# Kernel optimization log

Measured on AMD Instinct MI355X. Metric: run time of the kernel, lower is better.

Reference implementation:

```python
import jax, jax.numpy as jnp
import numpy as np

# --- Cl(5,0) geometric algebra with 32 basis blades (bitmask representation) ---
def _cayley():
    def sgn(a, b):
        # sign from reordering basis vectors (Euclidean metric: no metric signs)
        a >>= 1
        s = 0
        while a:
            s += bin(a & b).count('1')
            a >>= 1
        return -1.0 if (s & 1) else 1.0
    C = np.zeros((32, 32, 32), np.float32)
    for i in range(32):
        for j in range(32):
            C[i, j, i ^ j] = sgn(i, j)
    return jnp.asarray(C)

CAYLEY = _cayley()  # [32,32,32] structure constants
EPS = 1e-8

def geometric_product(a, b):
    # a, b: [..., 32]
    return jnp.einsum('...i,...j,ijk->...k', a, b, CAYLEY)

def manifold_normalization(x):
    # project multivector back to the unit-norm manifold
    return x * jax.lax.rsqrt(jnp.sum(x * x, axis=-1, keepdims=True) + EPS)


def setup_inputs() -> dict:
    key = jax.random.key(0)
    k1, k2, k3 = jax.random.split(key, 3)
    B, S, N, D = 16, 256, 16, 6
    H = 16  # hidden_channels
    x = jax.random.normal(k1, (B, S, N, D), dtype=jnp.float32)
    W_in = jax.random.normal(k2, (D, H * 32), dtype=jnp.float32) * 0.1
    b_in = jnp.zeros((H * 32,), dtype=jnp.float32)
    W_out = jax.random.normal(k3, (H * 32, D), dtype=jnp.float32) * 0.05
    b_out = jnp.zeros((D,), dtype=jnp.float32)
    return {"x": x, "W_in": W_in, "b_in": b_in, "W_out": W_out, "b_out": b_out}


def reference(x, W_in, b_in, W_out, b_out):
    B, S, N, D = x.shape
    H = W_in.shape[1] // 32
    # proj_in over the whole sequence at once
    x_embs = (x @ W_in + b_in).reshape(B, S, N, H, 32)
    # psi init: identity rotor (scalar blade = 1)
    psi0 = jnp.zeros((B, N, H, 32), dtype=x.dtype).at[..., 0].set(1.0)

    def step(psi, inp):
        u_t, x_t = inp  # [B,N,H,32], [B,N,D]
        delta_r = manifold_normalization(u_t.at[..., 0].add(1.0))
        psi = manifold_normalization(geometric_product(delta_r, psi))
        pred_delta = psi.reshape(B, N, H * 32) @ W_out + b_out
        return psi, x_t + pred_delta

    _, ys = jax.lax.scan(step, psi0,
                         (jnp.swapaxes(x_embs, 0, 1), jnp.swapaxes(x, 0, 1)))
    return jnp.swapaxes(ys, 0, 1)  # [B,S,N,D]
```

## Files before the change

### kernel.cpp

```cpp
#include <hip/hip_runtime.h>


#define EPS 1e-8f

constexpr int pcnt(int v) { int s = 0; while (v) { s += v & 1; v >>= 1; } return s; }
constexpr int sgni(int a, int b) {
    a >>= 1; int s = 0;
    while (a) { s += pcnt(a & b); a >>= 1; }
    return (s & 1) ? -1 : 1;
}
struct El { int m; int s; };
constexpr El emul(El a, El b) { return { a.m ^ b.m, a.s * b.s * sgni(a.m, b.m) }; }

struct MTab {
    int mm[16]; int ms[16];
    int qi[4][4]; int qs[4][4];
    int sig[32];
    bool ok;
};
constexpr MTab mkMT() {
    MTab t{}; t.ok = true;
    El g0{17,1}, g1{18,1}, g2{20,1}, g3{24,1};
    El q1 = emul(g0, g1), q2 = emul(g1, g2);
    El q[4] = { El{0,1}, q1, q2, emul(q1, q2) };
    El u = emul(emul(g0, g1), emul(g2, g3));
    El v = emul(emul(g0, g1), g2);
    El mset[4] = { El{0,1}, u, v, emul(u, v) };
    {
        El c1 = emul(q[1], q[1]); if (!(c1.m == 0 && c1.s == -1)) t.ok = false;
        El c2 = emul(q[2], q[2]); if (!(c2.m == 0 && c2.s == -1)) t.ok = false;
        El c3 = emul(q[3], q[3]); if (!(c3.m == 0 && c3.s == -1)) t.ok = false;
        El c4 = emul(u, u); if (!(c4.m == 0 && c4.s == 1)) t.ok = false;
        El c5 = emul(v, v); if (!(c5.m == 0 && c5.s == 1)) t.ok = false;
        El c6 = emul(u, v), c7 = emul(v, u);
        if (!(c6.m == c7.m && c6.s == -c7.s)) t.ok = false;
        for (int i = 1; i < 4; ++i) {
            El a1 = emul(u, q[i]), a2 = emul(q[i], u);
            if (!(a1.m == a2.m && a1.s == a2.s)) t.ok = false;
            El b1 = emul(v, q[i]), b2 = emul(q[i], v);
            if (!(b1.m == b2.m && b1.s == b2.s)) t.ok = false;
        }
    }
    for (int tt = 0; tt < 4; ++tt)
        for (int a = 0; a < 4; ++a) {
            El e = emul(q[a], mset[tt]);
            t.mm[a + 4 * tt] = e.m; t.ms[a + 4 * tt] = e.s;
            if (pcnt(e.m) & 1) t.ok = false;
        }
    for (int i = 0; i < 16; ++i)
        for (int j = i + 1; j < 16; ++j)
            if (t.mm[i] == t.mm[j]) t.ok = false;
    for (int a = 0; a < 4; ++a)
        for (int b = 0; b < 4; ++b) {
            El e = emul(q[a], q[b]);
            int f = -1;
            for (int c = 0; c < 4; ++c) if (q[c].m == e.m) f = c;
            if (f < 0) { t.ok = false; f = 0; }
            t.qi[a][b] = f; t.qs[a][b] = e.s * q[f].s;
        }
    for (int m = 0; m < 32; ++m) t.sig[m] = sgni(m ^ 31, 31);
    return t;
}
__device__ constexpr MTab MT = mkMT();
static_assert(mkMT().ok, "Cl(5,0) = M2(H)+M2(H) derivation failed");

__global__ __launch_bounds__(256, 1) void k_prep(
        const float* __restrict__ W_in, const float* __restrict__ b_in,
        const float* __restrict__ W_out, float* __restrict__ WP) {
    const int idx = blockIdx.x * 256 + threadIdx.x;
    if (idx >= 6656) return;
    if (idx < 3584) {
        const int h = idx / 224, r = idx % 224;
        const int es = r / 112, r2 = r % 112;
        const float p = es ? -1.f : 1.f;
        const int c = (r2 < 96) ? (r2 & 15) : (r2 - 96);
        const int e = c >> 2, a = c & 3;
        const int base = (e == 0 || e == 3) ? 0 : 8;
        const float se = (e == 0 || e == 1) ? 1.f : -1.f;
        float val = 0.f;
        for (int k = 0; k < 2; ++k) {
            const int i = a + base + 4 * k;
            const float beta = k ? se : 1.f;
            const int m = MT.mm[i];
            const float s = (float)MT.ms[i];
            const float sg = (float)MT.sig[m];
            float wm, wn;
            if (r2 < 96) {
                const int d = r2 >> 4;
                wm = W_in[d * 512 + h * 32 + m];
                wn = W_in[d * 512 + h * 32 + (m ^ 31)];
            } else {
                wm = b_in[h * 32 + m];
                wn = b_in[h * 32 + (m ^ 31)];
            }
            val += beta * s * (wm + p * sg * wn);
        }
        WP[idx] = val;
    } else {
        const int j = idx - 3584;
        const int h = j / 192, r = j % 192;
        const int es = r / 96, r2 = r % 96;
        const float p = es ? -1.f : 1.f;
        const int c = r2 / 6, d = r2 % 6;
        const int e = c >> 2, a = c & 3;
        const int base = (e == 0 || e == 3) ? 0 : 8;
        const float se = (e == 0 || e == 1) ? 1.f : -1.f;
        float val = 0.f;
        for (int k = 0; k < 2; ++k) {
            const int i = a + base + 4 * k;
            const float beta = k ? se : 1.f;
            const int m = MT.mm[i];
            const float s = (float)MT.ms[i];
            const float sg = (float)MT.sig[m];
            const float wm = W_out[(h * 32 + m) * 6 + d];
            const float wn = W_out[(h * 32 + (m ^ 31)) * 6 + d];
            val += 0.25f * beta * s * (wm + p * sg * wn);
        }
        WP[idx] = val;
    }
}

__device__ __forceinline__ void build16(const float* __restrict__ Wsp,
                                        const float xv[6], float U[16]) {
#pragma unroll
    for (int c = 0; c < 16; ++c) U[c] = Wsp[96 + c];
#pragma unroll
    for (int d = 0; d < 6; ++d)
#pragma unroll
        for (int c = 0; c < 16; ++c)
            U[c] = fmaf(xv[d], Wsp[d * 16 + c], U[c]);
    U[0]  += 1.0f;
    U[12] += 1.0f;
}

__device__ __forceinline__ void hfma(float* __restrict__ z,
                                     const float* __restrict__ p,
                                     const float* __restrict__ q) {
#pragma unroll
    for (int a = 0; a < 4; ++a)
#pragma unroll
        for (int b = 0; b < 4; ++b)
            z[MT.qi[a][b]] = fmaf((float)MT.qs[a][b] * p[a], q[b], z[MT.qi[a][b]]);
}

__device__ __forceinline__ void gpm(float* __restrict__ Z,
                                    const float* __restrict__ U,
                                    const float* __restrict__ X) {
#pragma unroll
    for (int k = 0; k < 16; ++k) Z[k] = 0.f;
    hfma(Z + 0,  U + 0, X + 0);   hfma(Z + 0,  U + 4,  X + 8);
    hfma(Z + 4,  U + 0, X + 4);   hfma(Z + 4,  U + 4,  X + 12);
    hfma(Z + 8,  U + 8, X + 0);   hfma(Z + 8,  U + 12, X + 8);
    hfma(Z + 12, U + 8, X + 4);   hfma(Z + 12, U + 12, X + 12);
}

__device__ __forceinline__ float ssum32(const float* a, const float* b) {
    float s0 = 0.f, s1 = 0.f, s2 = 0.f, s3 = 0.f;
#pragma unroll
    for (int k = 0; k < 16; k += 4) {
        s0 = fmaf(a[k],     a[k],     s0); s1 = fmaf(a[k + 1], a[k + 1], s1);
        s2 = fmaf(a[k + 2], a[k + 2], s2); s3 = fmaf(a[k + 3], a[k + 3], s3);
        s0 = fmaf(b[k],     b[k],     s0); s1 = fmaf(b[k + 1], b[k + 1], s1);
        s2 = fmaf(b[k + 2], b[k + 2], s2); s3 = fmaf(b[k + 3], b[k + 3], s3);
    }
    return (s0 + s1) + (s2 + s3);
}

__global__ __launch_bounds__(256, 1) void k_fused(
        const float* __restrict__ x, const float* __restrict__ WP,
        float* __restrict__ WS4) {
    __shared__ float LP[4 * 8 * 64 * 6];

    const int tid  = threadIdx.x;
    const int lane = tid & 63;
    const int w    = __builtin_amdgcn_readfirstlane((int)(tid >> 6));
    const int hg   = blockIdx.x & 3;
    const int p    = blockIdx.x >> 2;
    const int h    = 4 * hg + w;
    const int sc   = lane & 31;
    const int bn = p * 2 + (lane >> 5), b = bn >> 4, n = bn & 15;
    const float* __restrict__ Wp0 = WP + h * 224;
    const float* __restrict__ Wp1 = WP + h * 224 + 112;
    const float* __restrict__ Op0 = WP + 3584 + h * 192;
    const float* __restrict__ Op1 = WP + 3584 + h * 192 + 96;

    float Xp[16], Xm[16];
    {
        const int t = sc * 8;
        const float2* xp = (const float2*)(x + ((b * 256 + t) * 16 + n) * 6);
        float2 x01 = xp[0], x23 = xp[1], x45 = xp[2];
        const float xv[6] = {x01.x, x01.y, x23.x, x23.y, x45.x, x45.y};
        build16(Wp0, xv, Xp);
        build16(Wp1, xv, Xm);
    }
    for (int i = 1; i < 8; ++i) {
        const int t = sc * 8 + i;
        const float2* xp = (const float2*)(x + ((b * 256 + t) * 16 + n) * 6);
        float2 x01 = xp[0], x23 = xp[1], x45 = xp[2];
        const float xv[6] = {x01.x, x01.y, x23.x, x23.y, x45.x, x45.y};
        float U[16], Z[16];
        build16(Wp0, xv, U);
        gpm(Z, U, Xp);
#pragma unroll
        for (int k = 0; k < 16; ++k) Xp[k] = Z[k];
        build16(Wp1, xv, U);
        gpm(Z, U, Xm);
#pragma unroll
        for (int k = 0; k < 16; ++k) Xm[k] = Z[k];
    }
    {
        float rs = rsqrtf(0.25f * ssum32(Xp, Xm) + EPS);
#pragma unroll
        for (int k = 0; k < 16; ++k) { Xp[k] *= rs; Xm[k] *= rs; }
    }

#pragma unroll
    for (int k = 1; k < 32; k <<= 1) {
        float prp[16], prm[16];
#pragma unroll
        for (int j = 0; j < 16; ++j) {
            prp[j] = __shfl_up(Xp[j], k, 32);
            prm[j] = __shfl_up(Xm[j], k, 32);
        }
        if (sc >= k) {
            float Z[16];
            gpm(Z, Xp, prp);
#pragma unroll
            for (int m = 0; m < 16; ++m) Xp[m] = Z[m];
            gpm(Z, Xm, prm);
#pragma unroll
            for (int m = 0; m < 16; ++m) Xm[m] = Z[m];
        }
    }
    {
        float rs = rsqrtf(0.25f * ssum32(Xp, Xm) + EPS);
#pragma unroll
        for (int j = 0; j < 16; ++j) { Xp[j] *= rs; Xm[j] *= rs; }
    }
    float Rp[16], Rm[16];
#pragma unroll
    for (int j = 0; j < 16; ++j) {
        Rp[j] = __shfl_up(Xp[j], 1, 32);
        Rm[j] = __shfl_up(Xm[j], 1, 32);
    }
    if (sc == 0) {
#pragma unroll
        for (int j = 0; j < 16; ++j) { Rp[j] = 0.0f; Rm[j] = 0.0f; }
        Rp[0] = 1.0f; Rp[12] = 1.0f;
        Rm[0] = 1.0f; Rm[12] = 1.0f;
    }

    for (int i = 0; i < 8; ++i) {
        const int t = sc * 8 + i;
        const float2* xp = (const float2*)(x + ((b * 256 + t) * 16 + n) * 6);
        float2 x01 = xp[0], x23 = xp[1], x45 = xp[2];
        const float xv[6] = {x01.x, x01.y, x23.x, x23.y, x45.x, x45.y};
        float U[16], Zp[16], Zm[16];
        build16(Wp0, xv, U);
        gpm(Zp, U, Rp);
        build16(Wp1, xv, U);
        gpm(Zm, U, Rm);
        float rs = rsqrtf(0.25f * ssum32(Zp, Zm) + EPS);
        float pd[6] = {0.f, 0.f, 0.f, 0.f, 0.f, 0.f};
#pragma unroll
        for (int c = 0; c < 16; ++c)
#pragma unroll
            for (int d = 0; d < 6; ++d) {
                pd[d] = fmaf(Zp[c], Op0[c * 6 + d], pd[d]);
                pd[d] = fmaf(Zm[c], Op1[c * 6 + d], pd[d]);
            }
#pragma unroll
        for (int k = 0; k < 16; ++k) { Rp[k] = Zp[k]; Rm[k] = Zm[k]; }
        float* lp = LP + ((w * 8 + i) * 64 + lane) * 6;
#pragma unroll
        for (int d = 0; d < 6; ++d) lp[d] = pd[d] * rs;
    }

    __syncthreads();

    float* outp = WS4 + (hg * 128 + p) * 3072;
    for (int s = tid; s < 3072; s += 256) {
        const int d = s % 6, tc = s / 6;
        const int c = tc & 1, t = tc >> 1;
        const int li = ((t & 7) * 64 + (c * 32 + (t >> 3))) * 6 + d;
        float acc = LP[0 * 3072 + li] + LP[1 * 3072 + li]
                  + LP[2 * 3072 + li] + LP[3 * 3072 + li];
        outp[s] = acc;
    }
}

__global__ __launch_bounds__(256, 1) void k_reduce(
        const float* __restrict__ x, const float* __restrict__ b_out,
        const float* __restrict__ WS4, float* __restrict__ out) {
    const int idx = blockIdx.x * 256 + threadIdx.x;
    const int p = idx / 3072, s = idx % 3072;
    const int d = s % 6, tc = s / 6;
    const int c = tc & 1, t = tc >> 1;
    const int bn = p * 2 + c, b = bn >> 4, n = bn & 15;
    const int o = ((b * 256 + t) * 16 + n) * 6 + d;
    float acc = x[o] + b_out[d];
#pragma unroll
    for (int hg = 0; hg < 4; ++hg)
        acc += WS4[(hg * 128 + p) * 3072 + s];
    out[o] = acc;
}

extern "C" void kernel_launch(void* const* d_in, const int* in_sizes, int n_in,
                              void* d_out, int out_size, void* d_ws, size_t ws_size,
                              hipStream_t stream) {
    (void)in_sizes; (void)n_in; (void)out_size; (void)ws_size;
    const float* x     = (const float*)d_in[0];
    const float* W_in  = (const float*)d_in[1];
    const float* b_in  = (const float*)d_in[2];
    const float* W_out = (const float*)d_in[3];
    const float* b_out = (const float*)d_in[4];
    float* out = (float*)d_out;

    float* WP  = (float*)d_ws;
    float* WS4 = (float*)((char*)d_ws + 32768);

    k_prep  <<<26,   256, 0, stream>>>(W_in, b_in, W_out, WP);
    k_fused <<<512,  256, 0, stream>>>(x, WP, WS4);
    k_reduce<<<1536, 256, 0, stream>>>(x, b_out, WS4, out);
}
```

Measured before the change: 119.4 us.

## Replace workspace reduction kernel with atomic accumulation into output

Removes the separate reduce kernel and the partial-sum workspace. The prep kernel is widened to also initialise the output with x plus b_out. The fused kernel then atomically adds its per-head-group partial sums directly into the output. The shared-memory layout is transposed so each lane's six outputs are stored with a stride of 64 to reduce bank conflicts. This saves one launch and a workspace round trip, at the cost of four-way atomic contention per output element and nondeterministic summation order.

```diff
diff --git a/kernel.cpp b/kernel.cpp
--- a/kernel.cpp
+++ b/kernel.cpp
@@ -66,8 +66,11 @@
 
 __global__ __launch_bounds__(256, 1) void k_prep(
         const float* __restrict__ W_in, const float* __restrict__ b_in,
-        const float* __restrict__ W_out, float* __restrict__ WP) {
+        const float* __restrict__ W_out, const float* __restrict__ x,
+        const float* __restrict__ b_out, float* __restrict__ WP,
+        float* __restrict__ out) {
     const int idx = blockIdx.x * 256 + threadIdx.x;
+    if (idx < 393216) out[idx] = x[idx] + b_out[idx % 6];
     if (idx >= 6656) return;
     if (idx < 3584) {
         const int h = idx / 224, r = idx % 224;
@@ -168,8 +171,8 @@
 
 __global__ __launch_bounds__(256, 1) void k_fused(
         const float* __restrict__ x, const float* __restrict__ WP,
-        float* __restrict__ WS4) {
-    __shared__ float LP[4 * 8 * 64 * 6];
+        float* __restrict__ out) {
+    __shared__ float LP[4 * 8 * 6 * 64];
 
     const int tid  = threadIdx.x;
     const int lane = tid & 63;
@@ -271,38 +274,29 @@
             }
 #pragma unroll
         for (int k = 0; k < 16; ++k) { Rp[k] = Zp[k]; Rm[k] = Zm[k]; }
-        float* lp = LP + ((w * 8 + i) * 64 + lane) * 6;
-#pragma unroll
-        for (int d = 0; d < 6; ++d) lp[d] = pd[d] * rs;
+        float* lp = LP + ((w * 8 + i) * 6) * 64 + lane;
+#pragma unroll
+        for (int d = 0; d < 6; ++d) lp[d * 64] = pd[d] * rs;
     }
 
     __syncthreads();
 
-    float* outp = WS4 + (hg * 128 + p) * 3072;
-    for (int s = tid; s < 3072; s += 256) {
-        const int d = s % 6, tc = s / 6;
-        const int c = tc & 1, t = tc >> 1;
-        const int li = ((t & 7) * 64 + (c * 32 + (t >> 3))) * 6 + d;
-        float acc = LP[0 * 3072 + li] + LP[1 * 3072 + li]
-                  + LP[2 * 3072 + li] + LP[3 * 3072 + li];
-        outp[s] = acc;
-    }
-}
-
-__global__ __launch_bounds__(256, 1) void k_reduce(
-        const float* __restrict__ x, const float* __restrict__ b_out,
-        const float* __restrict__ WS4, float* __restrict__ out) {
-    const int idx = blockIdx.x * 256 + threadIdx.x;
-    const int p = idx / 3072, s = idx % 3072;
-    const int d = s % 6, tc = s / 6;
-    const int c = tc & 1, t = tc >> 1;
-    const int bn = p * 2 + c, b = bn >> 4, n = bn & 15;
-    const int o = ((b * 256 + t) * 16 + n) * 6 + d;
-    float acc = x[o] + b_out[d];
-#pragma unroll
-    for (int hg = 0; hg < 4; ++hg)
-        acc += WS4[(hg * 128 + p) * 3072 + s];
-    out[o] = acc;
+    {
+        const int c = lane >> 5;
+        const int bn2 = p * 2 + c, b2 = bn2 >> 4, n2 = bn2 & 15;
+        for (int t1 = 0; t1 < 2; ++t1) {
+            const int i = 2 * w + t1;
+            const int t = ((lane & 31) << 3) + i;
+            float* op = out + ((b2 * 256 + t) * 16 + n2) * 6;
+#pragma unroll
+            for (int d = 0; d < 6; ++d) {
+                const int li = (i * 6 + d) * 64 + lane;
+                float acc = LP[0 * 3072 + li] + LP[1 * 3072 + li]
+                          + LP[2 * 3072 + li] + LP[3 * 3072 + li];
+                unsafeAtomicAdd(op + d, acc);
+            }
+        }
+    }
 }
 
 extern "C" void kernel_launch(void* const* d_in, const int* in_sizes, int n_in,
@@ -316,10 +310,8 @@
     const float* b_out = (const float*)d_in[4];
     float* out = (float*)d_out;
 
-    float* WP  = (float*)d_ws;
-    float* WS4 = (float*)((char*)d_ws + 32768);
-
-    k_prep  <<<26,   256, 0, stream>>>(W_in, b_in, W_out, WP);
-    k_fused <<<512,  256, 0, stream>>>(x, WP, WS4);
-    k_reduce<<<1536, 256, 0, stream>>>(x, b_out, WS4, out);
-}
+    float* WP = (float*)d_ws;
+
+    k_prep <<<1536, 256, 0, stream>>>(W_in, b_in, W_out, x, b_out, WP, out);
+    k_fused<<<512,  256, 0, stream>>>(x, WP, out);
+}
```

Measured after the change: 155.7 us. +30.4%, slower.

## Drop weight-prep kernel; transform weights to eigen-basis on the fly

Applied to the files above, without the earlier changes.

Removes the k_prep launch that precomputed eigen-space (M2(H)+M2(H)) weight tables. The fused kernel now builds the full 32-blade embedding from the raw W_in/b_in and converts it to the Up/Um split inline. The output projection maps the split back to blades before multiplying by the raw W_out. This saves one kernel launch and its dependency, but roughly doubles the per-step embedding FMAs (32 outputs instead of 2x16) and adds transform arithmetic in the hot loops.

```diff
diff --git a/kernel.cpp b/kernel.cpp
--- a/kernel.cpp
+++ b/kernel.cpp
@@ -64,73 +64,92 @@
 __device__ constexpr MTab MT = mkMT();
 static_assert(mkMT().ok, "Cl(5,0) = M2(H)+M2(H) derivation failed");
 
-__global__ __launch_bounds__(256, 1) void k_prep(
-        const float* __restrict__ W_in, const float* __restrict__ b_in,
-        const float* __restrict__ W_out, float* __restrict__ WP) {
-    const int idx = blockIdx.x * 256 + threadIdx.x;
-    if (idx >= 6656) return;
-    if (idx < 3584) {
-        const int h = idx / 224, r = idx % 224;
-        const int es = r / 112, r2 = r % 112;
-        const float p = es ? -1.f : 1.f;
-        const int c = (r2 < 96) ? (r2 & 15) : (r2 - 96);
-        const int e = c >> 2, a = c & 3;
-        const int base = (e == 0 || e == 3) ? 0 : 8;
-        const float se = (e == 0 || e == 1) ? 1.f : -1.f;
-        float val = 0.f;
-        for (int k = 0; k < 2; ++k) {
-            const int i = a + base + 4 * k;
-            const float beta = k ? se : 1.f;
-            const int m = MT.mm[i];
-            const float s = (float)MT.ms[i];
-            const float sg = (float)MT.sig[m];
-            float wm, wn;
-            if (r2 < 96) {
-                const int d = r2 >> 4;
-                wm = W_in[d * 512 + h * 32 + m];
-                wn = W_in[d * 512 + h * 32 + (m ^ 31)];
-            } else {
-                wm = b_in[h * 32 + m];
-                wn = b_in[h * 32 + (m ^ 31)];
-            }
-            val += beta * s * (wm + p * sg * wn);
-        }
-        WP[idx] = val;
-    } else {
-        const int j = idx - 3584;
-        const int h = j / 192, r = j % 192;
-        const int es = r / 96, r2 = r % 96;
-        const float p = es ? -1.f : 1.f;
-        const int c = r2 / 6, d = r2 % 6;
-        const int e = c >> 2, a = c & 3;
-        const int base = (e == 0 || e == 3) ? 0 : 8;
-        const float se = (e == 0 || e == 1) ? 1.f : -1.f;
-        float val = 0.f;
-        for (int k = 0; k < 2; ++k) {
-            const int i = a + base + 4 * k;
-            const float beta = k ? se : 1.f;
-            const int m = MT.mm[i];
-            const float s = (float)MT.ms[i];
-            const float sg = (float)MT.sig[m];
-            const float wm = W_out[(h * 32 + m) * 6 + d];
-            const float wn = W_out[(h * 32 + (m ^ 31)) * 6 + d];
-            val += 0.25f * beta * s * (wm + p * sg * wn);
-        }
-        WP[idx] = val;
-    }
-}
-
-__device__ __forceinline__ void build16(const float* __restrict__ Wsp,
-                                        const float xv[6], float U[16]) {
-#pragma unroll
-    for (int c = 0; c < 16; ++c) U[c] = Wsp[96 + c];
+struct VTab {
+    int M0[16], M0X[16], M1[16], M1X[16];
+    float F0[16], G0[16], F1[16], G1[16];
+    int RM[16], RMX[16];
+    float RS[16], RSX[16];
+};
+constexpr VTab mkVT() {
+    VTab t{};
+    MTab mt = mkMT();
+    for (int c = 0; c < 16; ++c) {
+        int e = c >> 2, a = c & 3;
+        int base = (e == 0 || e == 3) ? 0 : 8;
+        int se = (e == 0 || e == 1) ? 1 : -1;
+        int i0 = a + base, i1 = i0 + 4;
+        t.M0[c] = mt.mm[i0]; t.M0X[c] = mt.mm[i0] ^ 31;
+        t.M1[c] = mt.mm[i1]; t.M1X[c] = mt.mm[i1] ^ 31;
+        t.F0[c] = (float)mt.ms[i0];
+        t.G0[c] = (float)(mt.ms[i0] * mt.sig[mt.mm[i0]]);
+        t.F1[c] = (float)(se * mt.ms[i1]);
+        t.G1[c] = (float)(se * mt.ms[i1] * mt.sig[mt.mm[i1]]);
+    }
+    for (int i = 0; i < 16; ++i) {
+        t.RM[i] = mt.mm[i]; t.RMX[i] = mt.mm[i] ^ 31;
+        t.RS[i] = (float)mt.ms[i];
+        t.RSX[i] = (float)(mt.sig[mt.mm[i]] * mt.ms[i]);
+    }
+    return t;
+}
+__device__ constexpr VTab VT = mkVT();
+
+constexpr bool verifyVT() {
+    MTab mt = mkMT();
+    for (int m = 0; m < 32; ++m) {
+        int V[32] = {}; V[m] = 1;
+        int Up[16] = {}, Um[16] = {};
+        for (int c = 0; c < 16; ++c) {
+            int e = c >> 2, a = c & 3;
+            int base = (e == 0 || e == 3) ? 0 : 8;
+            int se = (e == 0 || e == 1) ? 1 : -1;
+            int i0 = a + base, i1 = i0 + 4;
+            int m0 = mt.mm[i0], m1 = mt.mm[i1];
+            int f0 = mt.ms[i0], g0 = f0 * mt.sig[m0];
+            int f1 = se * mt.ms[i1], g1 = f1 * mt.sig[m1];
+            int a0 = f0 * V[m0], b0 = g0 * V[m0 ^ 31];
+            int a1 = f1 * V[m1], b1 = g1 * V[m1 ^ 31];
+            Up[c] = a0 + b0 + a1 + b1;
+            Um[c] = a0 - b0 + a1 - b1;
+        }
+        int r4[32] = {};
+        for (int i = 0; i < 16; ++i) {
+            int tt = i >> 2, a = i & 3;
+            int e1 = (tt < 2) ? 0 : 1, e2 = (tt < 2) ? 3 : 2;
+            int sg = (tt == 1 || tt == 3) ? -1 : 1;
+            int cp = Up[e1 * 4 + a] + sg * Up[e2 * 4 + a];
+            int cm = Um[e1 * 4 + a] + sg * Um[e2 * 4 + a];
+            int ev = cp + cm, od = cp - cm;
+            r4[mt.mm[i]] += mt.ms[i] * ev;
+            r4[mt.mm[i] ^ 31] += mt.sig[mt.mm[i]] * mt.ms[i] * od;
+        }
+        for (int k = 0; k < 32; ++k)
+            if (r4[k] != (k == m ? 4 : 0)) return false;
+    }
+    return true;
+}
+static_assert(verifyVT(), "on-the-fly eigen-transform roundtrip failed");
+
+__device__ __forceinline__ void build_es(const float* __restrict__ Wh,
+                                         const float* __restrict__ Bh,
+                                         const float xv[6],
+                                         float Up[16], float Um[16]) {
+    float V[32];
+#pragma unroll
+    for (int m = 0; m < 32; ++m) V[m] = Bh[m];
 #pragma unroll
     for (int d = 0; d < 6; ++d)
 #pragma unroll
-        for (int c = 0; c < 16; ++c)
-            U[c] = fmaf(xv[d], Wsp[d * 16 + c], U[c]);
-    U[0]  += 1.0f;
-    U[12] += 1.0f;
+        for (int m = 0; m < 32; ++m)
+            V[m] = fmaf(xv[d], Wh[d * 512 + m], V[m]);
+    V[0] += 1.0f;
+#pragma unroll
+    for (int c = 0; c < 16; ++c) {
+        const float a0 = VT.F0[c] * V[VT.M0[c]], b0 = VT.G0[c] * V[VT.M0X[c]];
+        const float a1 = VT.F1[c] * V[VT.M1[c]], b1 = VT.G1[c] * V[VT.M1X[c]];
+        Up[c] = (a0 + b0) + (a1 + b1);
+        Um[c] = (a0 - b0) + (a1 - b1);
+    }
 }
 
 __device__ __forceinline__ void hfma(float* __restrict__ z,
@@ -167,7 +186,8 @@
 }
 
 __global__ __launch_bounds__(256, 1) void k_fused(
-        const float* __restrict__ x, const float* __restrict__ WP,
+        const float* __restrict__ x, const float* __restrict__ W_in,
+        const float* __restrict__ b_in, const float* __restrict__ W_out,
         float* __restrict__ WS4) {
     __shared__ float LP[4 * 8 * 64 * 6];
 
@@ -179,10 +199,9 @@
     const int h    = 4 * hg + w;
     const int sc   = lane & 31;
     const int bn = p * 2 + (lane >> 5), b = bn >> 4, n = bn & 15;
-    const float* __restrict__ Wp0 = WP + h * 224;
-    const float* __restrict__ Wp1 = WP + h * 224 + 112;
-    const float* __restrict__ Op0 = WP + 3584 + h * 192;
-    const float* __restrict__ Op1 = WP + 3584 + h * 192 + 96;
+    const float* __restrict__ Wh = W_in  + h * 32;
+    const float* __restrict__ Bh = b_in  + h * 32;
+    const float* __restrict__ Wo = W_out + h * 192;
 
     float Xp[16], Xm[16];
     {
@@ -190,21 +209,19 @@
         const float2* xp = (const float2*)(x + ((b * 256 + t) * 16 + n) * 6);
         float2 x01 = xp[0], x23 = xp[1], x45 = xp[2];
         const float xv[6] = {x01.x, x01.y, x23.x, x23.y, x45.x, x45.y};
-        build16(Wp0, xv, Xp);
-        build16(Wp1, xv, Xm);
+        build_es(Wh, Bh, xv, Xp, Xm);
     }
     for (int i = 1; i < 8; ++i) {
         const int t = sc * 8 + i;
         const float2* xp = (const float2*)(x + ((b * 256 + t) * 16 + n) * 6);
         float2 x01 = xp[0], x23 = xp[1], x45 = xp[2];
         const float xv[6] = {x01.x, x01.y, x23.x, x23.y, x45.x, x45.y};
-        float U[16], Z[16];
-        build16(Wp0, xv, U);
-        gpm(Z, U, Xp);
+        float Up[16], Um[16], Z[16];
+        build_es(Wh, Bh, xv, Up, Um);
+        gpm(Z, Up, Xp);
 #pragma unroll
         for (int k = 0; k < 16; ++k) Xp[k] = Z[k];
-        build16(Wp1, xv, U);
-        gpm(Z, U, Xm);
+        gpm(Z, Um, Xm);
 #pragma unroll
         for (int k = 0; k < 16; ++k) Xm[k] = Z[k];
     }
@@ -255,20 +272,29 @@
         const float2* xp = (const float2*)(x + ((b * 256 + t) * 16 + n) * 6);
         float2 x01 = xp[0], x23 = xp[1], x45 = xp[2];
         const float xv[6] = {x01.x, x01.y, x23.x, x23.y, x45.x, x45.y};
-        float U[16], Zp[16], Zm[16];
-        build16(Wp0, xv, U);
-        gpm(Zp, U, Rp);
-        build16(Wp1, xv, U);
-        gpm(Zm, U, Rm);
-        float rs = rsqrtf(0.25f * ssum32(Zp, Zm) + EPS);
+        float Up[16], Um[16], Zp[16], Zm[16];
+        build_es(Wh, Bh, xv, Up, Um);
+        gpm(Zp, Up, Rp);
+        gpm(Zm, Um, Rm);
+        float rs = 0.25f * rsqrtf(0.25f * ssum32(Zp, Zm) + EPS);
         float pd[6] = {0.f, 0.f, 0.f, 0.f, 0.f, 0.f};
 #pragma unroll
-        for (int c = 0; c < 16; ++c)
+        for (int i16 = 0; i16 < 16; ++i16) {
+            const int tt = i16 >> 2, a = i16 & 3;
+            const int e1 = (tt < 2) ? 0 : 1, e2 = (tt < 2) ? 3 : 2;
+            const float sg = (tt == 1 || tt == 3) ? -1.f : 1.f;
+            const float cp = Zp[e1 * 4 + a] + sg * Zp[e2 * 4 + a];
+            const float cm = Zm[e1 * 4 + a] + sg * Zm[e2 * 4 + a];
+            const float ev = VT.RS[i16]  * (cp + cm);
+            const float od = VT.RSX[i16] * (cp - cm);
+            const float* wm = Wo + VT.RM[i16]  * 6;
+            const float* wx = Wo + VT.RMX[i16] * 6;
 #pragma unroll
             for (int d = 0; d < 6; ++d) {
-                pd[d] = fmaf(Zp[c], Op0[c * 6 + d], pd[d]);
-                pd[d] = fmaf(Zm[c], Op1[c * 6 + d], pd[d]);
+                pd[d] = fmaf(ev, wm[d], pd[d]);
+                pd[d] = fmaf(od, wx[d], pd[d]);
             }
+        }
 #pragma unroll
         for (int k = 0; k < 16; ++k) { Rp[k] = Zp[k]; Rm[k] = Zm[k]; }
         float* lp = LP + ((w * 8 + i) * 64 + lane) * 6;
@@ -316,10 +342,8 @@
     const float* b_out = (const float*)d_in[4];
     float* out = (float*)d_out;
 
-    float* WP  = (float*)d_ws;
-    float* WS4 = (float*)((char*)d_ws + 32768);
-
-    k_prep  <<<26,   256, 0, stream>>>(W_in, b_in, W_out, WP);
-    k_fused <<<512,  256, 0, stream>>>(x, WP, WS4);
+    float* WS4 = (float*)d_ws;
+
+    k_fused <<<512,  256, 0, stream>>>(x, W_in, b_in, W_out, WS4);
     k_reduce<<<1536, 256, 0, stream>>>(x, b_out, WS4, out);
 }
```

New measurement: 138.7 us. +16.2%, slower.
